# Optimization experiments

Hardware: AMD Instinct MI355X
Metric: run time of the kernel (lower is better)

Reference implementation:

```python
import jax, jax.numpy as jnp
import numpy as np

B, C, H, W = 2, 512, 64, 64


def conv1x1(x, w, b):
    # x: [B,C,H,W], w: [O,C], b: [O]
    return jnp.einsum('bchw,oc->bohw', x, w) + b[None, :, None, None]


def setup_inputs() -> dict:
    key = jax.random.key(0)
    ks = jax.random.split(key, 20)
    d = {
        'visSegF': jax.random.normal(ks[0], (B, C, H, W), jnp.float32),
        'irSegF': jax.random.normal(ks[1], (B, C, H, W), jnp.float32),
        'x_vis_p': jax.random.normal(ks[2], (B, C, H, W), jnp.float32),
        'x_ir_p': jax.random.normal(ks[3], (B, C, H, W), jnp.float32),
    }
    names = ['q_rd', 'k_rd', 'v_rd', 'q_dr', 'k_dr', 'v_dr']
    for i, n in enumerate(names):
        d['W' + n] = jax.random.normal(ks[4 + 2 * i], (C, C), jnp.float32) * 0.02
        d['b' + n] = jax.random.normal(ks[5 + 2 * i], (C,), jnp.float32) * 0.01
    # gamma params are init-zero in torch; use small nonzero values so both paths contribute
    d['gamma_rd'] = jax.random.normal(ks[16], (1,), jnp.float32) * 0.1
    d['gamma_dr'] = jax.random.normal(ks[17], (1,), jnp.float32) * 0.1
    return d


def reference(visSegF, irSegF, x_vis_p, x_ir_p,
              Wq_rd, bq_rd, Wk_rd, bk_rd, Wv_rd, bv_rd,
              Wq_dr, bq_dr, Wk_dr, bk_dr, Wv_dr, bv_dr,
              gamma_rd, gamma_dr):
    b, c, h, w = x_vis_p.shape
    n = h * w

    # rd path: query from x_vis_p, key from visSegF, value from x_ir_p (sr_ratio == 1 branch)
    q_vis = conv1x1(x_vis_p, Wq_rd, bq_rd).reshape(b, c, n)      # [B,C,N]
    key_d = conv1x1(visSegF, Wk_rd, bk_rd).reshape(b, c, -1)     # [B,C,M]
    val_d = conv1x1(x_ir_p, Wv_rd, bv_rd).reshape(b, c, -1)      # [B,C,M]
    # torch: softmax(bmm(q^T, k), dim=1) -> softmax over query positions (axis=1)
    attn_rd = jax.nn.softmax(jnp.einsum('bcn,bcm->bnm', q_vis, key_d), axis=1)
    out_rd = jnp.einsum('bcm,bnm->bcn', val_d, attn_rd).reshape(b, c, h, w)

    # dr path: query from x_ir_p, key/value from irSegF
    q_ir = conv1x1(x_ir_p, Wq_dr, bq_dr).reshape(b, c, n)
    key_r = conv1x1(irSegF, Wk_dr, bk_dr).reshape(b, c, -1)
    val_r = conv1x1(irSegF, Wv_dr, bv_dr).reshape(b, c, -1)
    attn_dr = jax.nn.softmax(jnp.einsum('bcn,bcm->bnm', q_ir, key_r), axis=1)
    out_dr = jnp.einsum('bcm,bnm->bcn', val_r, attn_dr).reshape(b, c, h, w)

    out_rd = jax.nn.relu(gamma_rd[0] * out_rd + x_vis_p)
    out_dr = jax.nn.relu(gamma_dr[0] * out_dr + x_ir_p)
    return (out_rd, out_dr)
```

## Files before the change

### kernel.cpp

```cpp
#include <hip/hip_runtime.h>
#include <stdint.h>


typedef __attribute__((ext_vector_type(8))) __bf16 bf16x8;
typedef __attribute__((ext_vector_type(4))) float f32x4;
typedef __attribute__((ext_vector_type(4))) unsigned short us4;

__device__ __forceinline__ unsigned short f2bf(float f) {
  union { float f; unsigned u; } v; v.f = f;
  unsigned r = v.u + 0x7FFFu + ((v.u >> 16) & 1u);
  return (unsigned short)(r >> 16);
}
__device__ __forceinline__ float bf2f(unsigned short b) {
  union { unsigned u; float f; } v; v.u = ((unsigned)b) << 16;
  return v.f;
}

__device__ __forceinline__ void async_copy16(const unsigned short* g,
                                             unsigned short* l) {
  __builtin_amdgcn_global_load_lds(
      (const __attribute__((address_space(1))) unsigned int*)g,
      (__attribute__((address_space(3))) unsigned int*)l, 16, 0, 0);
}

__device__ __forceinline__ void gemm_core(
    const unsigned short* __restrict__ Ag, const unsigned short* __restrict__ Bg,
    int K, int lda, int ldb, int rowbase, int colbase,
    f32x4 (&acc)[4][4], unsigned short* Al, unsigned short* Bl) {
  const int tid = threadIdx.x;
  const int w = tid >> 6, lane = tid & 63;
  const int quad = lane >> 4, l16 = lane & 15;
  const int wm = (w >> 1) << 6, wn = (w & 1) << 6;

  const int rbase = (w << 5) + (lane >> 2);

  for (int k0 = 0; k0 < K; k0 += 32) {
#pragma unroll
    for (int i = 0; i < 2; ++i) {
      int rloc = rbase + (i << 4);
      int cg = (lane & 3) ^ ((rloc >> 1) & 3);
      int koff = k0 + (cg << 3);
      int ldsoff = ((w << 5) + (i << 4)) << 5;
      async_copy16(Ag + (size_t)(rowbase + rloc) * lda + koff, Al + ldsoff);
      async_copy16(Bg + (size_t)(colbase + rloc) * ldb + koff, Bl + ldsoff);
    }
    __syncthreads();
    bf16x8 af[4], bfr[4];
#pragma unroll
    for (int i = 0; i < 4; ++i) {
      int r = wm + (i << 4) + l16;
      af[i] = *(const bf16x8*)(Al + (r << 5) + ((quad ^ ((r >> 1) & 3)) << 3));
    }
#pragma unroll
    for (int j = 0; j < 4; ++j) {
      int r = wn + (j << 4) + l16;
      bfr[j] = *(const bf16x8*)(Bl + (r << 5) + ((quad ^ ((r >> 1) & 3)) << 3));
    }
#pragma unroll
    for (int i = 0; i < 4; ++i)
#pragma unroll
      for (int j = 0; j < 4; ++j)
        acc[i][j] = __builtin_amdgcn_mfma_f32_16x16x32_bf16(af[i], bfr[j], acc[i][j], 0, 0, 0);
    __syncthreads();
  }
}

struct WArgs { const float* src[6]; unsigned short* dst[6]; };
__global__ __launch_bounds__(256) void k_cvtw(WArgs a) {
  int z = blockIdx.y;
  int i = blockIdx.x * 256 + threadIdx.x;
  a.dst[z][i] = f2bf(a.src[z][i]);
}

struct TArgs { const float* src[4]; unsigned short* dst[4]; };
__global__ __launch_bounds__(256) void k_tcvt(TArgs a) {
  __shared__ float tile[32][33];
  const float* src = a.src[blockIdx.z];
  unsigned short* dst = a.dst[blockIdx.z];
  int n0 = blockIdx.x << 5;
  int r0 = blockIdx.y << 5;
  int tx = threadIdx.x & 31, ty = threadIdx.x >> 5;
#pragma unroll
  for (int i = 0; i < 4; ++i)
    tile[ty * 4 + i][tx] = src[(size_t)(r0 + ty * 4 + i) * 4096 + n0 + tx];
  __syncthreads();
  int b = r0 >> 9, c0 = r0 & 511;
#pragma unroll
  for (int i = 0; i < 4; ++i) {
    int nn = ty * 4 + i;
    dst[(size_t)b * (4096 * 512) + (size_t)(n0 + nn) * 512 + c0 + tx] =
        f2bf(tile[tx][nn]);
  }
}

struct ConvArgs {
  const unsigned short* W[12];
  const unsigned short* X[12];
  const float* bias[12];
  unsigned short* out[12];
  int trans[12];
};
__global__ __launch_bounds__(256) void k_conv(ConvArgs a) {
  __shared__ unsigned short Al[128 * 32], Bl[128 * 32];
  int z = blockIdx.z;
  int rowbase = blockIdx.y << 7, colbase = blockIdx.x << 7;
  f32x4 acc[4][4];
#pragma unroll
  for (int i = 0; i < 4; ++i)
#pragma unroll
    for (int j = 0; j < 4; ++j) acc[i][j] = (f32x4){0.f, 0.f, 0.f, 0.f};
  gemm_core(a.W[z], a.X[z], 512, 512, 512, rowbase, colbase, acc, Al, Bl);

  const int tid = threadIdx.x, w = tid >> 6, lane = tid & 63;
  const int quad = lane >> 4, l16 = lane & 15;
  const int wm = (w >> 1) << 6, wn = (w & 1) << 6;
  const float* bias = a.bias[z];
  unsigned short* out = a.out[z];
  if (a.trans[z]) {
#pragma unroll
    for (int i = 0; i < 4; ++i) {
      int o0 = rowbase + wm + (i << 4) + (quad << 2);
      float b0 = bias[o0], b1 = bias[o0 + 1], b2 = bias[o0 + 2], b3 = bias[o0 + 3];
#pragma unroll
      for (int j = 0; j < 4; ++j) {
        int n = colbase + wn + (j << 4) + l16;
        us4 v;
        v.x = f2bf(acc[i][j].x + b0);
        v.y = f2bf(acc[i][j].y + b1);
        v.z = f2bf(acc[i][j].z + b2);
        v.w = f2bf(acc[i][j].w + b3);
        *(us4*)(out + (size_t)n * 512 + o0) = v;
      }
    }
  } else {
#pragma unroll
    for (int i = 0; i < 4; ++i) {
      int o0 = rowbase + wm + (i << 4) + (quad << 2);
      float b0 = bias[o0], b1 = bias[o0 + 1], b2 = bias[o0 + 2], b3 = bias[o0 + 3];
#pragma unroll
      for (int j = 0; j < 4; ++j) {
        int n = colbase + wn + (j << 4) + l16;
        out[(size_t)(o0 + 0) * 4096 + n] = f2bf(acc[i][j].x + b0);
        out[(size_t)(o0 + 1) * 4096 + n] = f2bf(acc[i][j].y + b1);
        out[(size_t)(o0 + 2) * 4096 + n] = f2bf(acc[i][j].z + b2);
        out[(size_t)(o0 + 3) * 4096 + n] = f2bf(acc[i][j].w + b3);
      }
    }
  }
}

struct QKArgs {
  const unsigned short* A[4]; const unsigned short* B[4]; unsigned short* T[4];
  float* pmx; float* pz;
};
__global__ __launch_bounds__(256) void k_qk(QKArgs a) {
  __shared__ unsigned short Al[128 * 32], Bl[128 * 32];
  int z = blockIdx.z;
  int rowbase = blockIdx.y << 7;
  int colbase = blockIdx.x << 7;
  f32x4 acc[4][4];
#pragma unroll
  for (int i = 0; i < 4; ++i)
#pragma unroll
    for (int j = 0; j < 4; ++j) acc[i][j] = (f32x4){0.f, 0.f, 0.f, 0.f};
  gemm_core(a.A[z], a.B[z], 512, 512, 512, rowbase, colbase, acc, Al, Bl);

  const int tid = threadIdx.x, w = tid >> 6, lane = tid & 63;
  const int quad = lane >> 4, l16 = lane & 15;
  const int wm = (w >> 1) << 6, wn = (w & 1) << 6;
  unsigned short* T = a.T[z];
#pragma unroll
  for (int i = 0; i < 4; ++i) {
    int m0 = rowbase + wm + (i << 4) + (quad << 2);
#pragma unroll
    for (int j = 0; j < 4; ++j) {
      int n = colbase + wn + (j << 4) + l16;
      us4 v;
      v.x = f2bf(__expf(acc[i][j].x));
      v.y = f2bf(__expf(acc[i][j].y));
      v.z = f2bf(__expf(acc[i][j].z));
      v.w = f2bf(__expf(acc[i][j].w));
      *(us4*)(T + (size_t)n * 4096 + m0) = v;
    }
  }
  float* red = (float*)Al;
#pragma unroll
  for (int i = 0; i < 4; ++i) {
#pragma unroll
    for (int r = 0; r < 4; ++r) {
      float lmax = fmaxf(fmaxf(acc[i][0][r], acc[i][1][r]),
                         fmaxf(acc[i][2][r], acc[i][3][r]));
#pragma unroll
      for (int d = 1; d < 16; d <<= 1) lmax = fmaxf(lmax, __shfl_xor(lmax, d, 64));
      float ls = 0.f;
#pragma unroll
      for (int j = 0; j < 4; ++j) ls += __expf(acc[i][j][r] - lmax);
#pragma unroll
      for (int d = 1; d < 16; d <<= 1) ls += __shfl_xor(ls, d, 64);
      if (l16 == 0) {
        int lr = (i << 4) + (quad << 2) + r;
        red[((w << 6) + lr) * 2 + 0] = lmax;
        red[((w << 6) + lr) * 2 + 1] = ls;
      }
    }
  }
  __syncthreads();
  if (tid < 128) {
    int wmh = tid >> 6, lr = tid & 63;
    float M0 = red[(((wmh << 1) + 0) * 64 + lr) * 2 + 0];
    float S0 = red[(((wmh << 1) + 0) * 64 + lr) * 2 + 1];
    float M1 = red[(((wmh << 1) + 1) * 64 + lr) * 2 + 0];
    float S1 = red[(((wmh << 1) + 1) * 64 + lr) * 2 + 1];
    float M = fmaxf(M0, M1);
    float S = S0 * __expf(M0 - M) + S1 * __expf(M1 - M);
    int m = rowbase + (wmh << 6) + lr;
    int idx = ((z << 5) + blockIdx.x) * 4096 + m;
    a.pmx[idx] = M;
    a.pz[idx] = S;
  }
}

__global__ __launch_bounds__(256) void k_stats2(const float* __restrict__ pmx,
                                                const float* __restrict__ pz,
                                                float* __restrict__ c) {
  int m = (blockIdx.x << 8) + threadIdx.x;
  int z = blockIdx.y;
  float M = -1e30f;
#pragma unroll
  for (int k = 0; k < 32; ++k) M = fmaxf(M, pmx[((z << 5) + k) * 4096 + m]);
  float S = 0.f;
#pragma unroll
  for (int k = 0; k < 32; ++k)
    S += pz[((z << 5) + k) * 4096 + m] * __expf(pmx[((z << 5) + k) * 4096 + m] - M);
  c[z * 4096 + m] = __expf(-M) / S;
}

struct VSArgs { unsigned short* V[4]; const float* c; };
__global__ __launch_bounds__(256) void k_vscale(VSArgs a) {
  int z = blockIdx.y;
  int t = blockIdx.x * 256 + threadIdx.x;
  int m0 = (t & 511) << 3;
  int row = t >> 9;
  unsigned short* p = a.V[z] + (size_t)row * 4096 + m0;
  const float* cz = a.c + z * 4096 + m0;
  int4 raw = *(const int4*)p;
  unsigned short* u = (unsigned short*)&raw;
#pragma unroll
  for (int j = 0; j < 8; ++j) u[j] = f2bf(bf2f(u[j]) * cz[j]);
  *(int4*)p = raw;
}

struct PVArgs {
  const unsigned short* V[4];
  const unsigned short* P[4];
  const float* resid[4];
  const float* gamma[4];
  float* out[4];
};
__global__ __launch_bounds__(256) void k_pv(PVArgs a) {
  __shared__ unsigned short Al[128 * 32], Bl[128 * 32];
  int z = blockIdx.z;
  int rowbase = blockIdx.y << 7;
  int colbase = blockIdx.x << 7;
  f32x4 acc[4][4];
#pragma unroll
  for (int i = 0; i < 4; ++i)
#pragma unroll
    for (int j = 0; j < 4; ++j) acc[i][j] = (f32x4){0.f, 0.f, 0.f, 0.f};
  gemm_core(a.V[z], a.P[z], 4096, 4096, 4096, rowbase, colbase, acc, Al, Bl);

  const int tid = threadIdx.x, w = tid >> 6, lane = tid & 63;
  const int quad = lane >> 4, l16 = lane & 15;
  const int wm = (w >> 1) << 6, wn = (w & 1) << 6;
  float g = a.gamma[z][0];
  const float* R = a.resid[z];
  float* O = a.out[z];
#pragma unroll
  for (int i = 0; i < 4; ++i) {
    int c0 = rowbase + wm + (i << 4) + (quad << 2);
#pragma unroll
    for (int j = 0; j < 4; ++j) {
      int n = colbase + wn + (j << 4) + l16;
      O[(size_t)(c0 + 0) * 4096 + n] = fmaxf(g * acc[i][j].x + R[(size_t)(c0 + 0) * 4096 + n], 0.f);
      O[(size_t)(c0 + 1) * 4096 + n] = fmaxf(g * acc[i][j].y + R[(size_t)(c0 + 1) * 4096 + n], 0.f);
      O[(size_t)(c0 + 2) * 4096 + n] = fmaxf(g * acc[i][j].z + R[(size_t)(c0 + 2) * 4096 + n], 0.f);
      O[(size_t)(c0 + 3) * 4096 + n] = fmaxf(g * acc[i][j].w + R[(size_t)(c0 + 3) * 4096 + n], 0.f);
    }
  }
}

extern "C" void kernel_launch(void* const* d_in, const int* in_sizes, int n_in,
                              void* d_out, int out_size, void* d_ws, size_t ws_size,
                              hipStream_t stream) {
  char* ws = (char*)d_ws;
  unsigned short* wb  = (unsigned short*)(ws);
  unsigned short* xt  = (unsigned short*)(ws + 3145728);
  unsigned short* qkv = (unsigned short*)(ws + 36700160);
  unsigned short* tt  = (unsigned short*)(ws + 87031808);
  float* pmx = (float*)(ws + 3145728);
  float* pz  = (float*)(ws + 3145728 + 2097152);
  float* cb  = (float*)(ws + 3145728 + 4194304);

  WArgs wa;
  for (int i = 0; i < 6; ++i) {
    wa.src[i] = (const float*)d_in[4 + 2 * i];
    wa.dst[i] = wb + (size_t)i * 262144;
  }
  k_cvtw<<<dim3(1024, 6), 256, 0, stream>>>(wa);

  TArgs ta;
  for (int ai = 0; ai < 4; ++ai) {
    ta.src[ai] = (const float*)d_in[ai];
    ta.dst[ai] = xt + (size_t)ai * 4194304;
  }
  k_tcvt<<<dim3(128, 32, 4), 256, 0, stream>>>(ta);

  const int srcArr[6] = {2, 0, 3, 3, 1, 1};
  const int trans[6] = {1, 1, 0, 1, 1, 0};
  ConvArgs ca;
  for (int ci = 0; ci < 6; ++ci)
    for (int b = 0; b < 2; ++b) {
      int zz = ci * 2 + b;
      ca.W[zz] = wb + (size_t)ci * 262144;
      ca.X[zz] = xt + (size_t)srcArr[ci] * 4194304 + (size_t)b * 2097152;
      ca.bias[zz] = (const float*)d_in[5 + 2 * ci];
      ca.out[zz] = qkv + (size_t)zz * 2097152;
      ca.trans[zz] = trans[ci];
    }
  k_conv<<<dim3(32, 4, 12), 256, 0, stream>>>(ca);

  QKArgs qa;
  for (int path = 0; path < 2; ++path)
    for (int b = 0; b < 2; ++b) {
      int zz = path * 2 + b;
      qa.A[zz] = qkv + (size_t)((path * 3 + 1) * 2 + b) * 2097152;
      qa.B[zz] = qkv + (size_t)((path * 3 + 0) * 2 + b) * 2097152;
      qa.T[zz] = tt + (size_t)zz * 16777216;
    }
  qa.pmx = pmx;
  qa.pz = pz;
  k_qk<<<dim3(32, 32, 4), 256, 0, stream>>>(qa);

  k_stats2<<<dim3(16, 4), 256, 0, stream>>>(pmx, pz, cb);

  VSArgs va;
  for (int path = 0; path < 2; ++path)
    for (int b = 0; b < 2; ++b)
      va.V[path * 2 + b] = qkv + (size_t)((path * 3 + 2) * 2 + b) * 2097152;
  va.c = cb;
  k_vscale<<<dim3(1024, 4), 256, 0, stream>>>(va);

  PVArgs pa;
  const float* resid_src[2] = {(const float*)d_in[2], (const float*)d_in[3]};
  const float* gsrc[2] = {(const float*)d_in[16], (const float*)d_in[17]};
  for (int path = 0; path < 2; ++path)
    for (int b = 0; b < 2; ++b) {
      int zz = path * 2 + b;
      pa.V[zz] = qkv + (size_t)((path * 3 + 2) * 2 + b) * 2097152;
      pa.P[zz] = tt + (size_t)zz * 16777216;
      pa.resid[zz] = resid_src[path] + (size_t)b * 2097152;
      pa.gamma[zz] = gsrc[path];
      pa.out[zz] = (float*)d_out + (size_t)path * 4194304 + (size_t)b * 2097152;
    }
  k_pv<<<dim3(32, 4, 4), 256, 0, stream>>>(pa);
}
```

Baseline: 442.9 us.

## Double GEMM K-step per barrier and drop max-tracking from softmax stats

The shared GEMM core now loads two 32-wide K slices into doubled LDS buffers per iteration, halving the number of barrier pairs across the K loop. The QK epilogue no longer computes per-row maxima; it accumulates raw exponential sums, and the stats kernel simply sums them and takes the reciprocal. This removes the max shuffles, extra exps and the pmx buffer traffic, at the cost of numerical safety if logits become large, and of doubled LDS use per block, which may reduce occupancy.

```diff
diff --git a/kernel.cpp b/kernel.cpp
--- a/kernel.cpp
+++ b/kernel.cpp
@@ -31,36 +31,46 @@
   const int w = tid >> 6, lane = tid & 63;
   const int quad = lane >> 4, l16 = lane & 15;
   const int wm = (w >> 1) << 6, wn = (w & 1) << 6;
-
   const int rbase = (w << 5) + (lane >> 2);
 
-  for (int k0 = 0; k0 < K; k0 += 32) {
-#pragma unroll
-    for (int i = 0; i < 2; ++i) {
-      int rloc = rbase + (i << 4);
-      int cg = (lane & 3) ^ ((rloc >> 1) & 3);
-      int koff = k0 + (cg << 3);
-      int ldsoff = ((w << 5) + (i << 4)) << 5;
-      async_copy16(Ag + (size_t)(rowbase + rloc) * lda + koff, Al + ldsoff);
-      async_copy16(Bg + (size_t)(colbase + rloc) * ldb + koff, Bl + ldsoff);
+  for (int k0 = 0; k0 < K; k0 += 64) {
+#pragma unroll
+    for (int half = 0; half < 2; ++half) {
+      int kh = k0 + (half << 5);
+      unsigned short* Ah = Al + (half << 12);
+      unsigned short* Bh = Bl + (half << 12);
+#pragma unroll
+      for (int i = 0; i < 2; ++i) {
+        int rloc = rbase + (i << 4);
+        int cg = (lane & 3) ^ ((rloc >> 1) & 3);
+        int koff = kh + (cg << 3);
+        int ldsoff = ((w << 5) + (i << 4)) << 5;
+        async_copy16(Ag + (size_t)(rowbase + rloc) * lda + koff, Ah + ldsoff);
+        async_copy16(Bg + (size_t)(colbase + rloc) * ldb + koff, Bh + ldsoff);
+      }
     }
     __syncthreads();
-    bf16x8 af[4], bfr[4];
-#pragma unroll
-    for (int i = 0; i < 4; ++i) {
-      int r = wm + (i << 4) + l16;
-      af[i] = *(const bf16x8*)(Al + (r << 5) + ((quad ^ ((r >> 1) & 3)) << 3));
-    }
-#pragma unroll
-    for (int j = 0; j < 4; ++j) {
-      int r = wn + (j << 4) + l16;
-      bfr[j] = *(const bf16x8*)(Bl + (r << 5) + ((quad ^ ((r >> 1) & 3)) << 3));
-    }
-#pragma unroll
-    for (int i = 0; i < 4; ++i)
-#pragma unroll
-      for (int j = 0; j < 4; ++j)
-        acc[i][j] = __builtin_amdgcn_mfma_f32_16x16x32_bf16(af[i], bfr[j], acc[i][j], 0, 0, 0);
+#pragma unroll
+    for (int half = 0; half < 2; ++half) {
+      unsigned short* Ah = Al + (half << 12);
+      unsigned short* Bh = Bl + (half << 12);
+      bf16x8 af[4], bfr[4];
+#pragma unroll
+      for (int i = 0; i < 4; ++i) {
+        int r = wm + (i << 4) + l16;
+        af[i] = *(const bf16x8*)(Ah + (r << 5) + ((quad ^ ((r >> 1) & 3)) << 3));
+      }
+#pragma unroll
+      for (int j = 0; j < 4; ++j) {
+        int r = wn + (j << 4) + l16;
+        bfr[j] = *(const bf16x8*)(Bh + (r << 5) + ((quad ^ ((r >> 1) & 3)) << 3));
+      }
+#pragma unroll
+      for (int i = 0; i < 4; ++i)
+#pragma unroll
+        for (int j = 0; j < 4; ++j)
+          acc[i][j] = __builtin_amdgcn_mfma_f32_16x16x32_bf16(af[i], bfr[j], acc[i][j], 0, 0, 0);
+    }
     __syncthreads();
   }
 }
@@ -101,7 +111,7 @@
   int trans[12];
 };
 __global__ __launch_bounds__(256) void k_conv(ConvArgs a) {
-  __shared__ unsigned short Al[128 * 32], Bl[128 * 32];
+  __shared__ unsigned short Al[2 * 128 * 32], Bl[2 * 128 * 32];
   int z = blockIdx.z;
   int rowbase = blockIdx.y << 7, colbase = blockIdx.x << 7;
   f32x4 acc[4][4];
@@ -151,10 +161,10 @@
 
 struct QKArgs {
   const unsigned short* A[4]; const unsigned short* B[4]; unsigned short* T[4];
-  float* pmx; float* pz;
+  float* pz;
 };
 __global__ __launch_bounds__(256) void k_qk(QKArgs a) {
-  __shared__ unsigned short Al[128 * 32], Bl[128 * 32];
+  __shared__ unsigned short Al[2 * 128 * 32], Bl[2 * 128 * 32];
   int z = blockIdx.z;
   int rowbase = blockIdx.y << 7;
   int colbase = blockIdx.x << 7;
@@ -169,70 +179,55 @@
   const int quad = lane >> 4, l16 = lane & 15;
   const int wm = (w >> 1) << 6, wn = (w & 1) << 6;
   unsigned short* T = a.T[z];
+  float* red = (float*)Al;
 #pragma unroll
   for (int i = 0; i < 4; ++i) {
     int m0 = rowbase + wm + (i << 4) + (quad << 2);
+    float rs0 = 0.f, rs1 = 0.f, rs2 = 0.f, rs3 = 0.f;
 #pragma unroll
     for (int j = 0; j < 4; ++j) {
       int n = colbase + wn + (j << 4) + l16;
+      float e0 = __expf(acc[i][j].x);
+      float e1 = __expf(acc[i][j].y);
+      float e2 = __expf(acc[i][j].z);
+      float e3 = __expf(acc[i][j].w);
       us4 v;
-      v.x = f2bf(__expf(acc[i][j].x));
-      v.y = f2bf(__expf(acc[i][j].y));
-      v.z = f2bf(__expf(acc[i][j].z));
-      v.w = f2bf(__expf(acc[i][j].w));
+      v.x = f2bf(e0); v.y = f2bf(e1); v.z = f2bf(e2); v.w = f2bf(e3);
       *(us4*)(T + (size_t)n * 4096 + m0) = v;
-    }
-  }
-  float* red = (float*)Al;
-#pragma unroll
-  for (int i = 0; i < 4; ++i) {
-#pragma unroll
-    for (int r = 0; r < 4; ++r) {
-      float lmax = fmaxf(fmaxf(acc[i][0][r], acc[i][1][r]),
-                         fmaxf(acc[i][2][r], acc[i][3][r]));
-#pragma unroll
-      for (int d = 1; d < 16; d <<= 1) lmax = fmaxf(lmax, __shfl_xor(lmax, d, 64));
-      float ls = 0.f;
-#pragma unroll
-      for (int j = 0; j < 4; ++j) ls += __expf(acc[i][j][r] - lmax);
-#pragma unroll
-      for (int d = 1; d < 16; d <<= 1) ls += __shfl_xor(ls, d, 64);
-      if (l16 == 0) {
-        int lr = (i << 4) + (quad << 2) + r;
-        red[((w << 6) + lr) * 2 + 0] = lmax;
-        red[((w << 6) + lr) * 2 + 1] = ls;
-      }
+      rs0 += e0; rs1 += e1; rs2 += e2; rs3 += e3;
+    }
+#pragma unroll
+    for (int d = 1; d < 16; d <<= 1) {
+      rs0 += __shfl_xor(rs0, d, 64);
+      rs1 += __shfl_xor(rs1, d, 64);
+      rs2 += __shfl_xor(rs2, d, 64);
+      rs3 += __shfl_xor(rs3, d, 64);
+    }
+    if (l16 == 0) {
+      int lr = (i << 4) + (quad << 2);
+      red[(w << 6) + lr + 0] = rs0;
+      red[(w << 6) + lr + 1] = rs1;
+      red[(w << 6) + lr + 2] = rs2;
+      red[(w << 6) + lr + 3] = rs3;
     }
   }
   __syncthreads();
   if (tid < 128) {
-    int wmh = tid >> 6, lr = tid & 63;
-    float M0 = red[(((wmh << 1) + 0) * 64 + lr) * 2 + 0];
-    float S0 = red[(((wmh << 1) + 0) * 64 + lr) * 2 + 1];
-    float M1 = red[(((wmh << 1) + 1) * 64 + lr) * 2 + 0];
-    float S1 = red[(((wmh << 1) + 1) * 64 + lr) * 2 + 1];
-    float M = fmaxf(M0, M1);
-    float S = S0 * __expf(M0 - M) + S1 * __expf(M1 - M);
-    int m = rowbase + (wmh << 6) + lr;
-    int idx = ((z << 5) + blockIdx.x) * 4096 + m;
-    a.pmx[idx] = M;
-    a.pz[idx] = S;
-  }
-}
-
-__global__ __launch_bounds__(256) void k_stats2(const float* __restrict__ pmx,
-                                                const float* __restrict__ pz,
+    int h = tid >> 6, lr = tid & 63;
+    float S = red[((h << 1) << 6) + lr] + red[(((h << 1) + 1) << 6) + lr];
+    int m = rowbase + (h << 6) + lr;
+    a.pz[((z << 5) + blockIdx.x) * 4096 + m] = S;
+  }
+}
+
+__global__ __launch_bounds__(256) void k_stats2(const float* __restrict__ pz,
                                                 float* __restrict__ c) {
   int m = (blockIdx.x << 8) + threadIdx.x;
   int z = blockIdx.y;
-  float M = -1e30f;
-#pragma unroll
-  for (int k = 0; k < 32; ++k) M = fmaxf(M, pmx[((z << 5) + k) * 4096 + m]);
   float S = 0.f;
 #pragma unroll
-  for (int k = 0; k < 32; ++k)
-    S += pz[((z << 5) + k) * 4096 + m] * __expf(pmx[((z << 5) + k) * 4096 + m] - M);
-  c[z * 4096 + m] = __expf(-M) / S;
+  for (int k = 0; k < 32; ++k) S += pz[((z << 5) + k) * 4096 + m];
+  c[z * 4096 + m] = 1.f / S;
 }
 
 struct VSArgs { unsigned short* V[4]; const float* c; };
@@ -258,7 +253,7 @@
   float* out[4];
 };
 __global__ __launch_bounds__(256) void k_pv(PVArgs a) {
-  __shared__ unsigned short Al[128 * 32], Bl[128 * 32];
+  __shared__ unsigned short Al[2 * 128 * 32], Bl[2 * 128 * 32];
   int z = blockIdx.z;
   int rowbase = blockIdx.y << 7;
   int colbase = blockIdx.x << 7;
@@ -297,9 +292,8 @@
   unsigned short* xt  = (unsigned short*)(ws + 3145728);
   unsigned short* qkv = (unsigned short*)(ws + 36700160);
   unsigned short* tt  = (unsigned short*)(ws + 87031808);
-  float* pmx = (float*)(ws + 3145728);
-  float* pz  = (float*)(ws + 3145728 + 2097152);
-  float* cb  = (float*)(ws + 3145728 + 4194304);
+  float* pz  = (float*)(ws + 3145728);
+  float* cb  = (float*)(ws + 3145728 + 2097152);
 
   WArgs wa;
   for (int i = 0; i < 6; ++i) {
@@ -337,11 +331,10 @@
       qa.B[zz] = qkv + (size_t)((path * 3 + 0) * 2 + b) * 2097152;
       qa.T[zz] = tt + (size_t)zz * 16777216;
     }
-  qa.pmx = pmx;
   qa.pz = pz;
   k_qk<<<dim3(32, 32, 4), 256, 0, stream>>>(qa);
 
-  k_stats2<<<dim3(16, 4), 256, 0, stream>>>(pmx, pz, cb);
+  k_stats2<<<dim3(16, 4), 256, 0, stream>>>(pz, cb);
 
   VSArgs va;
   for (int path = 0; path < 2; ++path)
```

Result: faster. 424.6 us (-4.1%).
